# Performance work log

Measured on AMD Instinct MI355X. Metric: run time of the kernel, lower is better.

The kernel has to match this reference:

```python
import jax, jax.numpy as jnp
import numpy as np
from jax.ops import segment_sum

N_NODES = 100000
N_EDGES = 3200000
DIM = 256
N_CLASSES = 32
N_GRAPHS = 64


def setup_inputs() -> dict:
    key = jax.random.key(0)
    k1, k2, k3, k4, k5 = jax.random.split(key, 5)
    x = jax.random.normal(k1, (N_NODES, DIM), dtype=jnp.float32)
    W = jax.random.normal(k2, (DIM, N_CLASSES), dtype=jnp.float32) / np.sqrt(DIM)
    b = jax.random.normal(k3, (N_CLASSES,), dtype=jnp.float32) * 0.01
    edge_index = jax.random.randint(k4, (2, N_EDGES), 0, N_NODES, dtype=jnp.int64)
    batch = jnp.sort(jax.random.randint(k5, (N_NODES,), 0, N_GRAPHS, dtype=jnp.int64))
    return {"x": x, "W": W, "b": b, "edge_index": edge_index, "batch": batch}


def reference(x, W, b, edge_index, batch):
    N = x.shape[0]
    # GCNConv: linear transform (no bias), then normalized aggregation, then bias
    h = x @ W  # [N, C]
    # add self loops (PyG default add_self_loops=True)
    loop = jnp.arange(N, dtype=edge_index.dtype)
    src = jnp.concatenate([edge_index[0], loop])  # source (message sender)
    dst = jnp.concatenate([edge_index[1], loop])  # target (aggregation site)
    # symmetric normalization: deg computed at target with unit edge weights
    deg = segment_sum(jnp.ones_like(dst, dtype=h.dtype), dst, num_segments=N)
    dinv = jnp.where(deg > 0, jax.lax.rsqrt(deg), 0.0)
    norm = dinv[src] * dinv[dst]  # [E+N]
    msg = h[src] * norm[:, None]  # gather + scale
    out = segment_sum(msg, dst, num_segments=N) + b  # scatter-add, bias after agg
    # global_mean_pool: segment mean over graphs
    cnt = segment_sum(jnp.ones((N,), dtype=out.dtype), batch, num_segments=N_GRAPHS)
    sums = segment_sum(out, batch, num_segments=N_GRAPHS)
    return sums / jnp.maximum(cnt, 1.0)[:, None]
```

## Files before the change

kernel.cpp:

```cpp
#include <hip/hip_runtime.h>

#define NN    100000
#define NE    3200000
#define DIMK  256
#define NC    32
#define NG    64

#define ROWS   64
#define NBUCK  1563
#define CAP    2432
#define NB1    512
#define EPB    6250
#define NSL    16
#define MAXG   512

static constexpr size_t OFF_REC    = 0;
static constexpr size_t OFF_DINV   = 15204864;
static constexpr size_t OFF_BTOT   = 15604864;
static constexpr size_t OFF_START  = 15613056;
static constexpr size_t OFF_CTRL   = 15613568;
static constexpr size_t OFF_P2     = 15613696;
static constexpr size_t OFF_PART   = 16662272;
static constexpr size_t OFF_NODEI  = OFF_PART;
static constexpr size_t OFF_CNT    = OFF_PART + 400000;
static constexpr size_t OFF_EXC    = OFF_PART + 3601024;

__device__ __forceinline__ int idx_at(const void* p, long i, bool i64) {
    return i64 ? (int)((const long long*)p)[i] : ((const int*)p)[i];
}

__device__ __forceinline__ bool detect_i64(const void* ei) {
    const int* w = (const int*)ei;
    return (w[1] == 0) & (w[3] == 0) & (w[5] == 0) &
           (w[7] == 0) & (w[9] == 0) & (w[11] == 0);
}

__global__ __launch_bounds__(256) void k_pre(const void* __restrict__ ei,
        unsigned int* __restrict__ parts, int* __restrict__ cnt) {
    __shared__ unsigned int h[12500];
    const bool i64 = detect_i64(ei);
    const int b = blockIdx.x;
    if (b < 256) {
        const int hh = b >> 7;
        const int sl = b & 127;
        const int lo = hh * 50000, hi = lo + 50000;
        for (int t = threadIdx.x; t < 12500; t += 256) h[t] = 0u;
        __syncthreads();
        const int e0 = sl * 25000;
        for (int e = e0 + threadIdx.x; e < e0 + 25000; e += 256) {
            int d = idx_at(ei, (long)NE + e, i64);
            if (d >= lo && d < hi) {
                int r = d - lo;
                atomicAdd(&h[r >> 2], 1u << ((r & 3) * 8));
            }
        }
        __syncthreads();
        for (int t = threadIdx.x; t < 12500; t += 256)
            parts[(size_t)b * 12500 + t] = h[t];
    } else {
        const int k = b - 256;
        for (int t = threadIdx.x; t < NBUCK; t += 256) h[t] = 0u;
        __syncthreads();
        const int e0 = k * EPB;
        for (int e = e0 + threadIdx.x; e < e0 + EPB; e += 256) {
            int s = idx_at(ei, e, i64);
            atomicAdd(&h[s >> 6], 1u);
        }
        __syncthreads();
        for (int t = threadIdx.x; t < NBUCK; t += 256)
            cnt[t * NB1 + k] = (int)h[t];
    }
}

__global__ __launch_bounds__(512) void k_mid(const unsigned int* __restrict__ parts,
        unsigned int* __restrict__ nodeinfo, float* __restrict__ dinv,
        const void* __restrict__ batch, const void* __restrict__ ei,
        int* __restrict__ start, const int* __restrict__ cnt,
        int* __restrict__ exc, int* __restrict__ btot) {
    __shared__ int s[512];
    const int b = blockIdx.x;
    const int t = threadIdx.x;
    if (b < 49) {
        const bool i64 = detect_i64(ei);
        int i = b * 512 + t;
        if (i >= 25000) return;
        int h = (i >= 12500) ? 1 : 0;
        int w = i - h * 12500;
        int c0 = 0, c1 = 0, c2 = 0, c3 = 0;
        const unsigned int* base = parts + (size_t)(h * 128) * 12500 + w;
#pragma unroll 4
        for (int q = 0; q < 128; ++q) {
            unsigned int v = base[(size_t)q * 12500];
            c0 += v & 255u; c1 += (v >> 8) & 255u; c2 += (v >> 16) & 255u; c3 += v >> 24;
        }
        int node = h * 50000 + w * 4;
        dinv[node]     = 1.0f / sqrtf((float)(1 + c0));
        dinv[node + 1] = 1.0f / sqrtf((float)(1 + c1));
        dinv[node + 2] = 1.0f / sqrtf((float)(1 + c2));
        dinv[node + 3] = 1.0f / sqrtf((float)(1 + c3));
        nodeinfo[node]     = ((unsigned)(1 + c0) << 6) | (unsigned)idx_at(batch, node, i64);
        nodeinfo[node + 1] = ((unsigned)(1 + c1) << 6) | (unsigned)idx_at(batch, node + 1, i64);
        nodeinfo[node + 2] = ((unsigned)(1 + c2) << 6) | (unsigned)idx_at(batch, node + 2, i64);
        nodeinfo[node + 3] = ((unsigned)(1 + c3) << 6) | (unsigned)idx_at(batch, node + 3, i64);
    } else if (b < 245) {
        const bool i64 = detect_i64(ei);
        int i = (b - 49) * 512 + t;
        if (i >= NN) return;
        int bi = idx_at(batch, i, i64);
        int bp = (i == 0) ? -1 : idx_at(batch, i - 1, i64);
        for (int g = bp + 1; g <= bi; ++g) start[g] = i;
        if (i == NN - 1)
            for (int g = bi + 1; g <= NG; ++g) start[g] = NN;
    } else {
        const int bkt = b - 245;
        int v = cnt[bkt * NB1 + t];
        s[t] = v;
        __syncthreads();
        for (int off = 1; off < 512; off <<= 1) {
            int u = (t >= off) ? s[t - off] : 0;
            __syncthreads();
            s[t] += u;
            __syncthreads();
        }
        exc[bkt * NB1 + t] = bkt * CAP + (s[t] - v);
        if (t == 511) btot[bkt] = s[511];
    }
}

__global__ __launch_bounds__(256) void k_place(const void* __restrict__ ei,
        const unsigned int* __restrict__ nodeinfo,
        const int* __restrict__ exc, unsigned int* __restrict__ rec,
        int* __restrict__ ctrl) {
    __shared__ unsigned int lc[NBUCK];
    __shared__ int lbase[NBUCK];
    const bool i64 = detect_i64(ei);
    const int k = blockIdx.x;
    if (k == 0 && threadIdx.x == 0) ctrl[1] = 0;
    for (int t = threadIdx.x; t < NBUCK; t += 256) {
        lc[t] = 0u;
        lbase[t] = exc[t * NB1 + k];
    }
    __syncthreads();
    const int e0 = k * EPB;
    for (int e = e0 + threadIdx.x; e < e0 + EPB; e += 256) {
        int s = idx_at(ei, e, i64);
        int d = idx_at(ei, (long)NE + e, i64);
        unsigned int ni = nodeinfo[d];
        unsigned int deg = min(ni >> 6, 1048575u);
        unsigned int g = ni & 63u;
        int b = s >> 6;
        unsigned int r = atomicAdd(&lc[b], 1u);
        rec[lbase[b] + (int)r] = (deg << 12) | (g * 64 + (unsigned)(s & 63));
    }
}

__global__ __launch_bounds__(512, 2) void k_fused(
        const float* __restrict__ x, const float* __restrict__ dinv,
        const void* __restrict__ batch, const void* __restrict__ ei,
        const unsigned int* __restrict__ rec, const int* __restrict__ btot,
        float* __restrict__ part, int* __restrict__ ctrl) {
    __shared__ __align__(16) float Ach[64 * ROWS];
    __shared__ int sbkt;
    const bool i64 = detect_i64(ei);
    const int tid  = threadIdx.x;
    const int gi   = tid >> 6;
    const int lane = tid & 63;

    float acc[8][4];
#pragma unroll
    for (int g = 0; g < 8; ++g)
#pragma unroll
        for (int d = 0; d < 4; ++d) acc[g][d] = 0.0f;

    const float4* x4 = (const float4*)x;
    float4* Ach4 = (float4*)Ach;
    const float4 z4 = make_float4(0.f, 0.f, 0.f, 0.f);
    const int jmax = NN - 1;

    for (;;) {
        if (tid == 0) sbkt = atomicAdd(&ctrl[1], 1);
        __syncthreads();
        const int bkt = sbkt;
        if (bkt >= NBUCK) break;
        const int j0 = bkt * ROWS;

        Ach4[tid] = z4;
        Ach4[tid + 512] = z4;
        __syncthreads();
        if (tid < ROWS) {
            int j = j0 + tid;
            if (j < NN) Ach[idx_at(batch, j, i64) * 64 + tid] = dinv[j];
        }
        __syncthreads();
        {
            const int rb = bkt * CAP;
            const int re = rb + btot[bkt];
            for (int r = rb + tid; r < re; r += 512) {
                unsigned int q = rec[r];
                float val = 1.0f / sqrtf((float)(q >> 12));
                atomicAdd(&Ach[q & 4095u], val);
            }
        }
        __syncthreads();
        float areg[8];
        {
            float dv = dinv[min(j0 + lane, jmax)];
#pragma unroll
            for (int q = 0; q < 8; ++q)
                areg[q] = Ach[(gi * 8 + q) * 64 + lane] * dv;
        }
        __syncthreads();

        if (bkt < NBUCK - 1) {
            const float4* xp = x4 + (size_t)j0 * 64 + lane;
            float4 buf[8];
#pragma unroll
            for (int k = 0; k < 8; ++k) buf[k] = xp[k * 64];
            xp += 512;
            for (int c = 0; c < 8; ++c) {
#pragma unroll
                for (int jj = 0; jj < 8; ++jj) {
                    float4 xv = buf[jj];
                    buf[jj] = xp[jj * 64];
#pragma unroll
                    for (int q = 0; q < 8; ++q) {
                        float aq = __int_as_float(__builtin_amdgcn_readlane(
                            __float_as_int(areg[q]), c * 8 + jj));
                        acc[q][0] = fmaf(aq, xv.x, acc[q][0]);
                        acc[q][1] = fmaf(aq, xv.y, acc[q][1]);
                        acc[q][2] = fmaf(aq, xv.z, acc[q][2]);
                        acc[q][3] = fmaf(aq, xv.w, acc[q][3]);
                    }
                }
                xp += 512;
                __syncthreads();
            }
        } else {
            float4 xv = x4[(size_t)min(j0, jmax) * 64 + lane];
#pragma unroll 4
            for (int jj = 0; jj < ROWS; ++jj) {
                float4 xn = x4[(size_t)min(j0 + jj + 1, jmax) * 64 + lane];
#pragma unroll
                for (int q = 0; q < 8; ++q) {
                    float aq = __int_as_float(__builtin_amdgcn_readlane(
                        __float_as_int(areg[q]), jj));
                    acc[q][0] = fmaf(aq, xv.x, acc[q][0]);
                    acc[q][1] = fmaf(aq, xv.y, acc[q][1]);
                    acc[q][2] = fmaf(aq, xv.z, acc[q][2]);
                    acc[q][3] = fmaf(aq, xv.w, acc[q][3]);
                }
                xv = xn;
            }
        }
    }

    float* p = part + (size_t)blockIdx.x * (NG * DIMK);
#pragma unroll
    for (int g = 0; g < 8; ++g) {
        float4 w = make_float4(acc[g][0], acc[g][1], acc[g][2], acc[g][3]);
        ((float4*)(p + (gi * 8 + g) * DIMK))[lane] = w;
    }
}

__global__ __launch_bounds__(256) void k_reduce1(const float4* __restrict__ part,
        float4* __restrict__ p2, int nblk) {
    int id = blockIdx.x * 256 + threadIdx.x;
    int c4 = id & 4095;
    int sl = id >> 12;
    int span = (nblk + NSL - 1) / NSL;
    int b0 = sl * span, b1 = min(b0 + span, nblk);
    float4 s = make_float4(0.f, 0.f, 0.f, 0.f);
    for (int b = b0; b < b1; ++b) {
        float4 v = part[(size_t)b * 4096 + c4];
        s.x += v.x; s.y += v.y; s.z += v.z; s.w += v.w;
    }
    p2[(size_t)sl * 4096 + c4] = s;
}

__global__ __launch_bounds__(256) void k_final(const float* __restrict__ p2,
        const float* __restrict__ W, const float* __restrict__ bias,
        const int* __restrict__ start, float* __restrict__ out) {
    __shared__ float Sb[8 * DIMK];
    const int tid = threadIdx.x, b = blockIdx.x;
    for (int t = tid; t < 8 * DIMK; t += 256) {
        int gl = t >> 8, d = t & 255;
        float s = 0.f;
#pragma unroll
        for (int sl = 0; sl < NSL; ++sl)
            s += p2[(size_t)sl * (NG * DIMK) + (b * 8 + gl) * DIMK + d];
        Sb[t] = s;
    }
    __syncthreads();
    int g = tid >> 5, c = tid & 31;
    float sum = 0.f;
#pragma unroll 8
    for (int d = 0; d < DIMK; ++d)
        sum = fmaf(Sb[g * DIMK + d], W[d * NC + c], sum);
    int gg = b * 8 + g;
    float cn = (float)max(start[gg + 1] - start[gg], 1);
    out[gg * NC + c] = sum / cn + bias[c];
}

extern "C" void kernel_launch(void* const* d_in, const int* in_sizes, int n_in,
                              void* d_out, int out_size, void* d_ws, size_t ws_size,
                              hipStream_t stream) {
    const float* x    = (const float*)d_in[0];
    const float* W    = (const float*)d_in[1];
    const float* bias = (const float*)d_in[2];
    const void*  ei   = d_in[3];
    const void*  batch= d_in[4];
    float* out = (float*)d_out;

    char* ws = (char*)d_ws;
    unsigned int* rec  = (unsigned int*)(ws + OFF_REC);
    unsigned int* degp = (unsigned int*)(ws + OFF_REC);
    float* dinv  = (float*)(ws + OFF_DINV);
    int*   btot  = (int*)(ws + OFF_BTOT);
    int*   start = (int*)(ws + OFF_START);
    int*   ctrl  = (int*)(ws + OFF_CTRL);
    float* p2    = (float*)(ws + OFF_P2);
    float* part  = (float*)(ws + OFF_PART);
    unsigned int* nodeinfo = (unsigned int*)(ws + OFF_NODEI);
    int*   cnt   = (int*)(ws + OFF_CNT);
    int*   exc   = (int*)(ws + OFF_EXC);

    long avail = (long)(ws_size - OFF_PART) / 65536;
    int grid = (int)avail;
    if (grid > MAXG) grid = MAXG;
    if (grid < 64) grid = 64;

    k_pre    <<<768, 256, 0, stream>>>(ei, degp, cnt);
    k_mid    <<<1808, 512, 0, stream>>>(degp, nodeinfo, dinv, batch, ei, start,
                                        cnt, exc, btot);
    k_place  <<<NB1, 256, 0, stream>>>(ei, nodeinfo, exc, rec, ctrl);
    k_fused  <<<grid, 512, 0, stream>>>(x, dinv, batch, ei, rec, btot, part, ctrl);
    k_reduce1<<<256, 256, 0, stream>>>((const float4*)part, (float4*)p2, grid);
    k_final  <<<8, 256, 0, stream>>>(p2, W, bias, start, out);
}
```

Baseline: 227.8 us.

## Split fused GEMM rows across wave halves and merge reduce kernels into one tail

The per-bucket work in k_fused is repartitioned. Each wave now owns 16 graph rows and handles half of the 64 node rows, instead of 8 graph rows over all 64 node rows, and the per-chunk __syncthreads inside the x streaming loop is removed. After the bucket loop the two halves are summed through shared memory before partials are written. k_reduce1 and k_final are merged into a single per-graph k_tail kernel, removing one launch and the p2 intermediate, at the cost of 16 accumulator rows per thread, which raises register pressure under launch_bounds(512,2).

```diff
diff --git a/kernel.cpp b/kernel.cpp
--- a/kernel.cpp
+++ b/kernel.cpp
@@ -11,7 +11,6 @@
 #define CAP    2432
 #define NB1    512
 #define EPB    6250
-#define NSL    16
 #define MAXG   512
 
 static constexpr size_t OFF_REC    = 0;
@@ -163,12 +162,15 @@
     __shared__ int sbkt;
     const bool i64 = detect_i64(ei);
     const int tid  = threadIdx.x;
-    const int gi   = tid >> 6;
+    const int w    = tid >> 6;
+    const int q    = w & 3;
+    const int rh   = w >> 2;
     const int lane = tid & 63;
-
-    float acc[8][4];
-#pragma unroll
-    for (int g = 0; g < 8; ++g)
+    const int rbase = rh << 5;
+
+    float acc[16][4];
+#pragma unroll
+    for (int g = 0; g < 16; ++g)
 #pragma unroll
         for (int d = 0; d < 4; ++d) acc[g][d] = 0.0f;
 
@@ -196,109 +198,120 @@
             const int rb = bkt * CAP;
             const int re = rb + btot[bkt];
             for (int r = rb + tid; r < re; r += 512) {
-                unsigned int q = rec[r];
-                float val = 1.0f / sqrtf((float)(q >> 12));
-                atomicAdd(&Ach[q & 4095u], val);
+                unsigned int qq = rec[r];
+                float val = 1.0f / sqrtf((float)(qq >> 12));
+                atomicAdd(&Ach[qq & 4095u], val);
             }
         }
         __syncthreads();
-        float areg[8];
+        float areg[16];
         {
             float dv = dinv[min(j0 + lane, jmax)];
 #pragma unroll
-            for (int q = 0; q < 8; ++q)
-                areg[q] = Ach[(gi * 8 + q) * 64 + lane] * dv;
+            for (int g = 0; g < 16; ++g)
+                areg[g] = Ach[(q * 16 + g) * 64 + lane] * dv;
         }
         __syncthreads();
 
         if (bkt < NBUCK - 1) {
-            const float4* xp = x4 + (size_t)j0 * 64 + lane;
+            const float4* xp = x4 + (size_t)(j0 + rbase) * 64 + lane;
             float4 buf[8];
 #pragma unroll
             for (int k = 0; k < 8; ++k) buf[k] = xp[k * 64];
             xp += 512;
-            for (int c = 0; c < 8; ++c) {
+            for (int c = 0; c < 4; ++c) {
 #pragma unroll
                 for (int jj = 0; jj < 8; ++jj) {
                     float4 xv = buf[jj];
                     buf[jj] = xp[jj * 64];
 #pragma unroll
-                    for (int q = 0; q < 8; ++q) {
+                    for (int g = 0; g < 16; ++g) {
                         float aq = __int_as_float(__builtin_amdgcn_readlane(
-                            __float_as_int(areg[q]), c * 8 + jj));
-                        acc[q][0] = fmaf(aq, xv.x, acc[q][0]);
-                        acc[q][1] = fmaf(aq, xv.y, acc[q][1]);
-                        acc[q][2] = fmaf(aq, xv.z, acc[q][2]);
-                        acc[q][3] = fmaf(aq, xv.w, acc[q][3]);
+                            __float_as_int(areg[g]), rbase + c * 8 + jj));
+                        acc[g][0] = fmaf(aq, xv.x, acc[g][0]);
+                        acc[g][1] = fmaf(aq, xv.y, acc[g][1]);
+                        acc[g][2] = fmaf(aq, xv.z, acc[g][2]);
+                        acc[g][3] = fmaf(aq, xv.w, acc[g][3]);
                     }
                 }
                 xp += 512;
-                __syncthreads();
             }
         } else {
-            float4 xv = x4[(size_t)min(j0, jmax) * 64 + lane];
 #pragma unroll 4
-            for (int jj = 0; jj < ROWS; ++jj) {
-                float4 xn = x4[(size_t)min(j0 + jj + 1, jmax) * 64 + lane];
-#pragma unroll
-                for (int q = 0; q < 8; ++q) {
+            for (int jj = 0; jj < 32; ++jj) {
+                float4 xv = x4[(size_t)min(j0 + rbase + jj, jmax) * 64 + lane];
+#pragma unroll
+                for (int g = 0; g < 16; ++g) {
                     float aq = __int_as_float(__builtin_amdgcn_readlane(
-                        __float_as_int(areg[q]), jj));
-                    acc[q][0] = fmaf(aq, xv.x, acc[q][0]);
-                    acc[q][1] = fmaf(aq, xv.y, acc[q][1]);
-                    acc[q][2] = fmaf(aq, xv.z, acc[q][2]);
-                    acc[q][3] = fmaf(aq, xv.w, acc[q][3]);
+                        __float_as_int(areg[g]), rbase + jj));
+                    acc[g][0] = fmaf(aq, xv.x, acc[g][0]);
+                    acc[g][1] = fmaf(aq, xv.y, acc[g][1]);
+                    acc[g][2] = fmaf(aq, xv.z, acc[g][2]);
+                    acc[g][3] = fmaf(aq, xv.w, acc[g][3]);
                 }
-                xv = xn;
             }
         }
     }
 
-    float* p = part + (size_t)blockIdx.x * (NG * DIMK);
-#pragma unroll
-    for (int g = 0; g < 8; ++g) {
-        float4 w = make_float4(acc[g][0], acc[g][1], acc[g][2], acc[g][3]);
-        ((float4*)(p + (gi * 8 + g) * DIMK))[lane] = w;
-    }
-}
-
-__global__ __launch_bounds__(256) void k_reduce1(const float4* __restrict__ part,
-        float4* __restrict__ p2, int nblk) {
-    int id = blockIdx.x * 256 + threadIdx.x;
-    int c4 = id & 4095;
-    int sl = id >> 12;
-    int span = (nblk + NSL - 1) / NSL;
-    int b0 = sl * span, b1 = min(b0 + span, nblk);
+    __syncthreads();
+#pragma unroll
+    for (int g = 0; g < 16; ++g) {
+        if (rh == 1)
+            Ach4[q * 64 + lane] = make_float4(acc[g][0], acc[g][1],
+                                              acc[g][2], acc[g][3]);
+        __syncthreads();
+        if (rh == 0) {
+            float4 v = Ach4[q * 64 + lane];
+            acc[g][0] += v.x; acc[g][1] += v.y;
+            acc[g][2] += v.z; acc[g][3] += v.w;
+        }
+        __syncthreads();
+    }
+
+    if (rh == 0) {
+        float* p = part + (size_t)blockIdx.x * (NG * DIMK);
+#pragma unroll
+        for (int g = 0; g < 16; ++g) {
+            float4 wv = make_float4(acc[g][0], acc[g][1], acc[g][2], acc[g][3]);
+            ((float4*)(p + (q * 16 + g) * DIMK))[lane] = wv;
+        }
+    }
+}
+
+__global__ __launch_bounds__(512) void k_tail(const float4* __restrict__ part,
+        const float* __restrict__ W, const float* __restrict__ bias,
+        const int* __restrict__ start, float* __restrict__ out, int nblk) {
+    __shared__ __align__(16) float4 ls[8][64];
+    __shared__ float Sb[DIMK];
+    const int tid = threadIdx.x, g = blockIdx.x;
+    const int c4 = tid & 63;
+    const int sl = tid >> 6;
     float4 s = make_float4(0.f, 0.f, 0.f, 0.f);
-    for (int b = b0; b < b1; ++b) {
-        float4 v = part[(size_t)b * 4096 + c4];
+    for (int b = sl; b < nblk; b += 8) {
+        float4 v = part[(size_t)b * 4096 + g * 64 + c4];
         s.x += v.x; s.y += v.y; s.z += v.z; s.w += v.w;
     }
-    p2[(size_t)sl * 4096 + c4] = s;
-}
-
-__global__ __launch_bounds__(256) void k_final(const float* __restrict__ p2,
-        const float* __restrict__ W, const float* __restrict__ bias,
-        const int* __restrict__ start, float* __restrict__ out) {
-    __shared__ float Sb[8 * DIMK];
-    const int tid = threadIdx.x, b = blockIdx.x;
-    for (int t = tid; t < 8 * DIMK; t += 256) {
-        int gl = t >> 8, d = t & 255;
-        float s = 0.f;
-#pragma unroll
-        for (int sl = 0; sl < NSL; ++sl)
-            s += p2[(size_t)sl * (NG * DIMK) + (b * 8 + gl) * DIMK + d];
-        Sb[t] = s;
-    }
+    ls[sl][c4] = s;
     __syncthreads();
-    int g = tid >> 5, c = tid & 31;
-    float sum = 0.f;
+    if (sl == 0) {
+        float4 t = ls[0][c4];
+#pragma unroll
+        for (int k = 1; k < 8; ++k) {
+            float4 v = ls[k][c4];
+            t.x += v.x; t.y += v.y; t.z += v.z; t.w += v.w;
+        }
+        Sb[c4 * 4 + 0] = t.x; Sb[c4 * 4 + 1] = t.y;
+        Sb[c4 * 4 + 2] = t.z; Sb[c4 * 4 + 3] = t.w;
+    }
+    __syncthreads();
+    if (tid < NC) {
+        float sum = 0.f;
 #pragma unroll 8
-    for (int d = 0; d < DIMK; ++d)
-        sum = fmaf(Sb[g * DIMK + d], W[d * NC + c], sum);
-    int gg = b * 8 + g;
-    float cn = (float)max(start[gg + 1] - start[gg], 1);
-    out[gg * NC + c] = sum / cn + bias[c];
+        for (int d = 0; d < DIMK; ++d)
+            sum = fmaf(Sb[d], W[d * NC + tid], sum);
+        float cn = (float)max(start[g + 1] - start[g], 1);
+        out[g * NC + tid] = sum / cn + bias[tid];
+    }
 }
 
 extern "C" void kernel_launch(void* const* d_in, const int* in_sizes, int n_in,
@@ -318,7 +331,6 @@
     int*   btot  = (int*)(ws + OFF_BTOT);
     int*   start = (int*)(ws + OFF_START);
     int*   ctrl  = (int*)(ws + OFF_CTRL);
-    float* p2    = (float*)(ws + OFF_P2);
     float* part  = (float*)(ws + OFF_PART);
     unsigned int* nodeinfo = (unsigned int*)(ws + OFF_NODEI);
     int*   cnt   = (int*)(ws + OFF_CNT);
@@ -329,11 +341,10 @@
     if (grid > MAXG) grid = MAXG;
     if (grid < 64) grid = 64;
 
-    k_pre    <<<768, 256, 0, stream>>>(ei, degp, cnt);
-    k_mid    <<<1808, 512, 0, stream>>>(degp, nodeinfo, dinv, batch, ei, start,
-                                        cnt, exc, btot);
-    k_place  <<<NB1, 256, 0, stream>>>(ei, nodeinfo, exc, rec, ctrl);
-    k_fused  <<<grid, 512, 0, stream>>>(x, dinv, batch, ei, rec, btot, part, ctrl);
-    k_reduce1<<<256, 256, 0, stream>>>((const float4*)part, (float4*)p2, grid);
-    k_final  <<<8, 256, 0, stream>>>(p2, W, bias, start, out);
-}
+    k_pre  <<<768, 256, 0, stream>>>(ei, degp, cnt);
+    k_mid  <<<1808, 512, 0, stream>>>(degp, nodeinfo, dinv, batch, ei, start,
+                                      cnt, exc, btot);
+    k_place<<<NB1, 256, 0, stream>>>(ei, nodeinfo, exc, rec, ctrl);
+    k_fused<<<grid, 512, 0, stream>>>(x, dinv, batch, ei, rec, btot, part, ctrl);
+    k_tail <<<NG, 512, 0, stream>>>((const float4*)part, W, bias, start, out, grid);
+}
```

Measured after the change: 219.2 us. -3.8%, faster.
